# Optimization experiments

Measured on AMD Instinct MI355X. Metric: run time of the kernel, lower is better.

The kernel has to match this reference:

```python
import jax, jax.numpy as jnp
import numpy as np

B, S, OBS, H, A, L = 512, 512, 64, 128, 9, 2
LN_EPS = 1e-5


def setup_inputs() -> dict:
    key = jax.random.key(0)
    ks = jax.random.split(key, 32)
    sc = 0.05
    inp = {
        'obs': jax.random.normal(ks[0], (B, S, OBS), jnp.float32),
        'masks': (jax.random.uniform(ks[1], (B, S)) > 0.01).astype(jnp.float32),
        'noise': jax.random.normal(ks[2], (B, S, A), jnp.float32),
        # encoder: Linear(OBS,H) -> LayerNorm(H) -> ReLU -> Linear(H,H) -> ReLU
        'enc_w1': jax.random.normal(ks[3], (H, OBS)) * sc,
        'enc_b1': jnp.zeros((H,)),
        'ln_g': jnp.ones((H,)),
        'ln_b': jnp.zeros((H,)),
        'enc_w2': jax.random.normal(ks[4], (H, H)) * sc,
        'enc_b2': jnp.zeros((H,)),
        # 2-layer LSTM, torch gate order [i, f, g, o]
        'wih0': jax.random.normal(ks[5], (4 * H, H)) * sc,
        'whh0': jax.random.normal(ks[6], (4 * H, H)) * sc,
        'bih0': jnp.zeros((4 * H,)),
        'bhh0': jnp.zeros((4 * H,)),
        'wih1': jax.random.normal(ks[7], (4 * H, H)) * sc,
        'whh1': jax.random.normal(ks[8], (4 * H, H)) * sc,
        'bih1': jnp.zeros((4 * H,)),
        'bhh1': jnp.zeros((4 * H,)),
        # actor mean head: Linear(H,H//2) -> ReLU -> Linear(H//2,A) -> Tanh
        'am_w1': jax.random.normal(ks[9], (H // 2, H)) * sc,
        'am_b1': jnp.zeros((H // 2,)),
        'am_w2': jax.random.normal(ks[10], (A, H // 2)) * sc,
        'am_b2': jnp.zeros((A,)),
        'log_std': jnp.full((A,), -1.0, jnp.float32),
        # critic head: Linear(H,H//2) -> ReLU -> Linear(H//2,1)
        'cr_w1': jax.random.normal(ks[11], (H // 2, H)) * sc,
        'cr_b1': jnp.zeros((H // 2,)),
        'cr_w2': jax.random.normal(ks[12], (1, H // 2)) * sc,
        'cr_b2': jnp.zeros((1,)),
    }
    return inp


def _encoder(x, w1, b1, g, b, w2, b2):
    y = x @ w1.T + b1
    mu = y.mean(-1, keepdims=True)
    var = y.var(-1, keepdims=True)
    y = (y - mu) * jax.lax.rsqrt(var + LN_EPS) * g + b
    y = jax.nn.relu(y)
    return jax.nn.relu(y @ w2.T + b2)


def _masked_lstm(enc, masks, wih, whh, bih, bhh):
    # enc: (B,S,H), masks: (B,S). Carry h,c: (L,B,H). Reset h,c by mask, then step.
    h0 = jnp.zeros((L, enc.shape[0], H), enc.dtype)
    c0 = jnp.zeros_like(h0)

    def step(carry, xs):
        h, c = carry
        x_t, m_t = xs  # (B,H), (B,1)
        h = h * m_t
        c = c * m_t
        hs, cs = [], []
        inp = x_t
        for l in range(L):
            gates = inp @ wih[l].T + bih[l] + h[l] @ whh[l].T + bhh[l]
            i, f, g, o = jnp.split(gates, 4, axis=-1)
            c_l = jax.nn.sigmoid(f) * c[l] + jax.nn.sigmoid(i) * jnp.tanh(g)
            h_l = jax.nn.sigmoid(o) * jnp.tanh(c_l)
            hs.append(h_l)
            cs.append(c_l)
            inp = h_l
        return (jnp.stack(hs), jnp.stack(cs)), inp

    xs = (enc.transpose(1, 0, 2), masks.T[:, :, None])  # time-major
    (h, c), outs = jax.lax.scan(step, (h0, c0), xs)
    return outs.transpose(1, 0, 2), h, c  # (B,S,H)


def reference(obs, masks, noise, enc_w1, enc_b1, ln_g, ln_b, enc_w2, enc_b2,
              wih0, whh0, bih0, bhh0, wih1, whh1, bih1, bhh1,
              am_w1, am_b1, am_w2, am_b2, log_std, cr_w1, cr_b1, cr_w2, cr_b2):
    enc = _encoder(obs, enc_w1, enc_b1, ln_g, ln_b, enc_w2, enc_b2)
    lstm_out, h, c = _masked_lstm(enc, masks, (wih0, wih1), (whh0, whh1),
                                  (bih0, bih1), (bhh0, bhh1))
    mean = jnp.tanh(jax.nn.relu(lstm_out @ am_w1.T + am_b1) @ am_w2.T + am_b2)
    ls = jnp.clip(log_std, -4.0, 0.0)
    std = jnp.exp(ls)
    action = jax.lax.stop_gradient(mean + std * noise)  # dist.sample()
    z = (action - mean) / std
    log_prob = (-0.5 * z * z - ls - 0.5 * jnp.log(2.0 * jnp.pi)).sum(-1)
    value = (jax.nn.relu(lstm_out @ cr_w1.T + cr_b1) @ cr_w2.T + cr_b2)[..., 0]
    return action, log_prob, value, h, c
```

## Files before the change

kernel.cpp:

```cpp
#include <hip/hip_runtime.h>
#include <hip/hip_bf16.h>
#include <math.h>


#define DEV __device__ __forceinline__

typedef __attribute__((ext_vector_type(4))) float f4;
typedef __attribute__((ext_vector_type(8))) short s16x8;

static constexpr int Bsz = 512, Ssz = 512, OBSD = 64, HD = 128, AD = 9;
static constexpr int TOK = Bsz * Ssz;

static constexpr size_t LP_OFF  = (size_t)TOK * AD;
static constexpr size_t VAL_OFF = LP_OFF + TOK;
static constexpr size_t H_OFF   = VAL_OFF + TOK;
static constexpr size_t C_OFF   = H_OFF + 2 * Bsz * HD;

static constexpr size_t WS_SEQ   = 0;
static constexpr size_t WS_WIH1B = (size_t)TOK * HD * 2;
static constexpr size_t WS_AMW1B = WS_WIH1B + 512 * 128 * 2;
static constexpr size_t WS_AMW2P = WS_AMW1B + 64 * 128 * 2;
static constexpr size_t WS_CRW1B = WS_AMW2P + 16 * 64 * 2;
static constexpr size_t WS_CRW2P = WS_CRW1B + 64 * 128 * 2;

DEV unsigned short f2bf(float f) {
  union { float f; unsigned u; } v; v.f = f;
  unsigned r = v.u + 0x7fffu + ((v.u >> 16) & 1u);
  return (unsigned short)(r >> 16);
}
DEV s16x8 cvt8(f4 a, f4 b) {
  s16x8 r;
  r[0]=(short)f2bf(a[0]); r[1]=(short)f2bf(a[1]); r[2]=(short)f2bf(a[2]); r[3]=(short)f2bf(a[3]);
  r[4]=(short)f2bf(b[0]); r[5]=(short)f2bf(b[1]); r[6]=(short)f2bf(b[2]); r[7]=(short)f2bf(b[3]);
  return r;
}
DEV f4 splat4(float v) { f4 r = {v, v, v, v}; return r; }
DEV f4 mfma16(s16x8 a, s16x8 b, f4 c) {
  return __builtin_amdgcn_mfma_f32_16x16x32_bf16(a, b, c, 0, 0, 0);
}
DEV float fexp2(float x) { return __builtin_amdgcn_exp2f(x); }
DEV float frcp(float x)  { return __builtin_amdgcn_rcpf(x); }
DEV float sigm(float x)   { return frcp(1.f + fexp2(-1.4426950408889634f * x)); }
DEV float tanh_f(float x) { return 2.f * frcp(1.f + fexp2(-2.8853900817779268f * x)) - 1.f; }

__global__ void k_prep(const float* __restrict__ wih1, const float* __restrict__ amw1,
                       const float* __restrict__ amw2, const float* __restrict__ crw1,
                       const float* __restrict__ crw2,
                       unsigned short* __restrict__ wih1b, unsigned short* __restrict__ amw1b,
                       unsigned short* __restrict__ amw2p, unsigned short* __restrict__ crw1b,
                       unsigned short* __restrict__ crw2p)
{
  int i = blockIdx.x * 256 + threadIdx.x;
  if (i < 65536) wih1b[i] = f2bf(wih1[i]);
  if (i < 8192) { amw1b[i] = f2bf(amw1[i]); crw1b[i] = f2bf(crw1[i]); }
  if (i < 1024) {
    int n = i >> 6, k = i & 63;
    amw2p[i] = (n < 9) ? f2bf(amw2[n * 64 + k]) : (unsigned short)0;
    crw2p[i] = (n == 0) ? f2bf(crw2[k]) : (unsigned short)0;
  }
}

__global__ __launch_bounds__(256) void k_encoder(
    const float* __restrict__ obs,
    const float* __restrict__ w1, const float* __restrict__ b1,
    const float* __restrict__ lng, const float* __restrict__ lnb,
    const float* __restrict__ w2, const float* __restrict__ b2,
    unsigned short* __restrict__ enc)
{
  __shared__ unsigned short sy[4][2048];
  const int tid = threadIdx.x, lane = tid & 63, wv = tid >> 6;
  const int cl = lane & 15, grp = lane >> 4;
  const size_t tok0 = ((size_t)blockIdx.x * 4 + wv) * 16;

  s16x8 aob[2];
  {
    const float* p = obs + (tok0 + cl) * 64 + grp * 8;
    aob[0] = cvt8(*(const f4*)p, *(const f4*)(p + 4));
    aob[1] = cvt8(*(const f4*)(p + 32), *(const f4*)(p + 36));
  }

  f4 acc[8];
#pragma unroll
  for (int n = 0; n < 8; ++n) acc[n] = splat4(0.f);
#pragma unroll
  for (int kk = 0; kk < 2; ++kk)
#pragma unroll
    for (int n = 0; n < 8; ++n) {
      const float* p = w1 + (size_t)(n * 16 + cl) * 64 + kk * 32 + grp * 8;
      acc[n] = mfma16(aob[kk], cvt8(*(const f4*)p, *(const f4*)(p + 4)), acc[n]);
    }

  float y[8][4], s[4] = {0,0,0,0}, q[4] = {0,0,0,0};
#pragma unroll
  for (int n = 0; n < 8; ++n) {
    float bb = b1[n * 16 + cl];
#pragma unroll
    for (int i = 0; i < 4; ++i) { float v = acc[n][i] + bb; y[n][i] = v; s[i] += v; q[i] += v * v; }
  }
#pragma unroll
  for (int i = 0; i < 4; ++i)
    for (int m = 1; m < 16; m <<= 1) { s[i] += __shfl_xor(s[i], m); q[i] += __shfl_xor(q[i], m); }
  float mean[4], rstd[4];
#pragma unroll
  for (int i = 0; i < 4; ++i) {
    mean[i] = s[i] * (1.f / 128.f);
    float var = q[i] * (1.f / 128.f) - mean[i] * mean[i];
    rstd[i] = rsqrtf(var + 1e-5f);
  }
  unsigned short* my = sy[wv];
#pragma unroll
  for (int n = 0; n < 8; ++n) {
    float gg = lng[n * 16 + cl], bb = lnb[n * 16 + cl];
#pragma unroll
    for (int i = 0; i < 4; ++i) {
      float v = (y[n][i] - mean[i]) * rstd[i] * gg + bb;
      v = v > 0.f ? v : 0.f;
      int row = grp * 4 + i;
      *(unsigned short*)((char*)my + row * 256 + (((n * 16 + cl) * 2) ^ ((row & 7) << 4))) = f2bf(v);
    }
  }
  __syncthreads();

  f4 acc2[8];
#pragma unroll
  for (int n = 0; n < 8; ++n) acc2[n] = splat4(0.f);
#pragma unroll
  for (int kk = 0; kk < 4; ++kk) {
    s16x8 a2 = *(const s16x8*)((char*)my + cl * 256 + ((kk * 64 + grp * 16) ^ ((cl & 7) << 4)));
#pragma unroll
    for (int n = 0; n < 8; ++n) {
      const float* p = w2 + (size_t)(n * 16 + cl) * 128 + kk * 32 + grp * 8;
      acc2[n] = mfma16(a2, cvt8(*(const f4*)p, *(const f4*)(p + 4)), acc2[n]);
    }
  }
#pragma unroll
  for (int n = 0; n < 8; ++n) {
    float bb = b2[n * 16 + cl];
#pragma unroll
    for (int i = 0; i < 4; ++i) {
      float v = acc2[n][i] + bb; v = v > 0.f ? v : 0.f;
      enc[(tok0 + grp * 4 + i) * 128 + n * 16 + cl] = f2bf(v);
    }
  }
}

__global__ __launch_bounds__(512, 2) void k_lstm(
    const unsigned short* enc_in,
    unsigned short* lstm_out,
    const float* __restrict__ masks,
    const float* __restrict__ wih0f, const float* __restrict__ whh0f,
    const float* __restrict__ bih0, const float* __restrict__ bhh0,
    const unsigned short* __restrict__ wih1b, const float* __restrict__ whh1f,
    const float* __restrict__ bih1, const float* __restrict__ bhh1,
    float* __restrict__ out_h, float* __restrict__ out_c)
{
  extern __shared__ char sm[];
  char* s_h0 = sm + 131072;
  char* s_h1 = sm + 135168;
  unsigned short* s_mk = (unsigned short*)(sm + 139264);

  const int tid = threadIdx.x, lane = tid & 63, wv = tid >> 6;
  const int cl = lane & 15, grp = lane >> 4;
  const int b0 = blockIdx.x * 16, u0 = wv * 16;
  const s16x8 z8 = {0,0,0,0,0,0,0,0};

  for (int idx = tid; idx < 8192; idx += 512) {
    int row = idx >> 4, c8 = idx & 15;
    const float* p = wih0f + (size_t)row * 128 + c8 * 8;
    s16x8 v = cvt8(*(const f4*)p, *(const f4*)(p + 4));
    *(s16x8*)(sm + row * 256 + ((c8 * 16) ^ ((row & 7) << 4))) = v;
  }
  for (int idx = tid; idx < 2048; idx += 512) { ((unsigned short*)s_h0)[idx] = 0; ((unsigned short*)s_h1)[idx] = 0; }
  for (int idx = tid; idx < 8192; idx += 512) {
    int t = idx >> 4, r = idx & 15;
    s_mk[idx] = (masks[(size_t)(b0 + r) * 512 + t] != 0.f) ? 1u : 0u;
  }

  s16x8 Bh0[4][4], Bh1[4][4];
#pragma unroll
  for (int g = 0; g < 4; ++g)
#pragma unroll
    for (int kk = 0; kk < 4; ++kk) {
      const float* p0 = whh0f + (size_t)(g * 128 + u0 + cl) * 128 + kk * 32 + grp * 8;
      Bh0[g][kk] = cvt8(*(const f4*)p0, *(const f4*)(p0 + 4));
      const float* p1 = whh1f + (size_t)(g * 128 + u0 + cl) * 128 + kk * 32 + grp * 8;
      Bh1[g][kk] = cvt8(*(const f4*)p1, *(const f4*)(p1 + 4));
    }
  float bias0[4], bias1[4];
#pragma unroll
  for (int g = 0; g < 4; ++g) {
    bias0[g] = bih0[g * 128 + u0 + cl] + bhh0[g * 128 + u0 + cl];
    bias1[g] = bih1[g * 128 + u0 + cl] + bhh1[g * 128 + u0 + cl];
  }
  float c0[4] = {0,0,0,0}, c1[4] = {0,0,0,0};
  float h0r[4] = {0,0,0,0}, h1r[4] = {0,0,0,0};

  const int swz = (cl & 7) << 4;
  int hoff[4];
#pragma unroll
  for (int kk = 0; kk < 4; ++kk) hoff[kk] = cl * 256 + ((kk * 64 + grp * 16) ^ swz);
  const char* w0l = sm + (u0 + cl) * 256;
  const unsigned short* encl = enc_in + (size_t)(b0 + cl) * 65536 + grp * 8;
  const unsigned short* w1l = wih1b + (size_t)(u0 + cl) * 128 + grp * 8;

  __syncthreads();

  for (int t = 0; t < 512; ++t) {
    const int mA = s_mk[t * 16 + cl];
    float mc[4];
#pragma unroll
    for (int i = 0; i < 4; ++i) mc[i] = s_mk[t * 16 + grp * 4 + i] ? 1.f : 0.f;

    f4 acc[4];
#pragma unroll
    for (int g = 0; g < 4; ++g) acc[g] = splat4(bias0[g]);
#pragma unroll
    for (int kk = 0; kk < 4; ++kk) {
      s16x8 ax = *(const s16x8*)(encl + (size_t)t * 128 + kk * 32);
      s16x8 ah = *(const s16x8*)(s_h0 + hoff[kk]);
      if (!mA) ah = z8;
#pragma unroll
      for (int g = 0; g < 4; ++g) {
        s16x8 bw = *(const s16x8*)(w0l + g * 32768 + ((kk * 64 + grp * 16) ^ swz));
        acc[g] = mfma16(ax, bw, acc[g]);
        acc[g] = mfma16(ah, Bh0[g][kk], acc[g]);
      }
    }
#pragma unroll
    for (int i = 0; i < 4; ++i) {
      float ig = sigm(acc[0][i]), fg = sigm(acc[1][i]);
      float gg = tanh_f(acc[2][i]), og = sigm(acc[3][i]);
      float c = fg * (c0[i] * mc[i]) + ig * gg;
      c0[i] = c; h0r[i] = og * tanh_f(c);
    }
    __syncthreads();
#pragma unroll
    for (int i = 0; i < 4; ++i) {
      int row = grp * 4 + i;
      *(unsigned short*)(s_h0 + row * 256 + (((u0 + cl) * 2) ^ ((row & 7) << 4))) = f2bf(h0r[i]);
    }
    __syncthreads();

#pragma unroll
    for (int g = 0; g < 4; ++g) acc[g] = splat4(bias1[g]);
    s16x8 ax1[4], ah1[4];
#pragma unroll
    for (int kk = 0; kk < 4; ++kk) {
      ax1[kk] = *(const s16x8*)(s_h0 + hoff[kk]);
      ah1[kk] = *(const s16x8*)(s_h1 + hoff[kk]);
      if (!mA) ah1[kk] = z8;
    }
#pragma unroll
    for (int g = 0; g < 4; ++g) {
#pragma unroll
      for (int kk = 0; kk < 4; ++kk) {
        s16x8 bx = *(const s16x8*)(w1l + g * 16384 + kk * 32);
        acc[g] = mfma16(ax1[kk], bx, acc[g]);
        acc[g] = mfma16(ah1[kk], Bh1[g][kk], acc[g]);
      }
    }
#pragma unroll
    for (int i = 0; i < 4; ++i) {
      float ig = sigm(acc[0][i]), fg = sigm(acc[1][i]);
      float gg = tanh_f(acc[2][i]), og = sigm(acc[3][i]);
      float c = fg * (c1[i] * mc[i]) + ig * gg;
      c1[i] = c; h1r[i] = og * tanh_f(c);
    }
    __syncthreads();
#pragma unroll
    for (int i = 0; i < 4; ++i) {
      int row = grp * 4 + i;
      unsigned short hb = f2bf(h1r[i]);
      *(unsigned short*)(s_h1 + row * 256 + (((u0 + cl) * 2) ^ ((row & 7) << 4))) = hb;
      lstm_out[(size_t)(b0 + row) * 65536 + (size_t)t * 128 + u0 + cl] = hb;
    }
    __syncthreads();
  }

#pragma unroll
  for (int i = 0; i < 4; ++i) {
    size_t b = (size_t)b0 + grp * 4 + i;
    out_h[b * 128 + u0 + cl]         = h0r[i];
    out_h[65536 + b * 128 + u0 + cl] = h1r[i];
    out_c[b * 128 + u0 + cl]         = c0[i];
    out_c[65536 + b * 128 + u0 + cl] = c1[i];
  }
}

__global__ __launch_bounds__(256) void k_heads(
    const unsigned short* __restrict__ lo,
    const float* __restrict__ noise,
    const unsigned short* __restrict__ amw1b, const float* __restrict__ am_b1,
    const unsigned short* __restrict__ amw2p, const float* __restrict__ am_b2,
    const float* __restrict__ log_std,
    const unsigned short* __restrict__ crw1b, const float* __restrict__ cr_b1,
    const unsigned short* __restrict__ crw2p, const float* __restrict__ cr_b2,
    float* __restrict__ out)
{
  __shared__ unsigned short sha[4][1024];
  __shared__ unsigned short shc[4][1024];
  const int tid = threadIdx.x, lane = tid & 63, wv = tid >> 6;
  const int cl = lane & 15, grp = lane >> 4;
  const size_t tok0 = ((size_t)blockIdx.x * 4 + wv) * 16;

  s16x8 a[4];
  {
    const unsigned short* p = lo + (tok0 + cl) * 128 + grp * 8;
#pragma unroll
    for (int kk = 0; kk < 4; ++kk) a[kk] = *(const s16x8*)(p + kk * 32);
  }

  f4 acc[4], accc[4];
#pragma unroll
  for (int n = 0; n < 4; ++n) { acc[n] = splat4(0.f); accc[n] = splat4(0.f); }
#pragma unroll
  for (int kk = 0; kk < 4; ++kk)
#pragma unroll
    for (int n = 0; n < 4; ++n) {
      acc[n]  = mfma16(a[kk], *(const s16x8*)(amw1b + (size_t)(n * 16 + cl) * 128 + kk * 32 + grp * 8), acc[n]);
      accc[n] = mfma16(a[kk], *(const s16x8*)(crw1b + (size_t)(n * 16 + cl) * 128 + kk * 32 + grp * 8), accc[n]);
    }
#pragma unroll
  for (int n = 0; n < 4; ++n) {
    float ba = am_b1[n * 16 + cl], bc = cr_b1[n * 16 + cl];
#pragma unroll
    for (int i = 0; i < 4; ++i) {
      int row = grp * 4 + i;
      int off = row * 128 + (((n * 16 + cl) * 2) ^ ((row & 7) << 4));
      float va = acc[n][i] + ba;  va = va > 0.f ? va : 0.f;
      float vc = accc[n][i] + bc; vc = vc > 0.f ? vc : 0.f;
      *(unsigned short*)((char*)sha[wv] + off) = f2bf(va);
      *(unsigned short*)((char*)shc[wv] + off) = f2bf(vc);
    }
  }
  __syncthreads();

  f4 am = splat4(0.f), vv = splat4(0.f);
#pragma unroll
  for (int kk = 0; kk < 2; ++kk) {
    int off = cl * 128 + ((kk * 64 + grp * 16) ^ ((cl & 7) << 4));
    s16x8 a2 = *(const s16x8*)((char*)sha[wv] + off);
    s16x8 c2 = *(const s16x8*)((char*)shc[wv] + off);
    am = mfma16(a2, *(const s16x8*)(amw2p + (size_t)cl * 64 + kk * 32 + grp * 8), am);
    vv = mfma16(c2, *(const s16x8*)(crw2p + (size_t)cl * 64 + kk * 32 + grp * 8), vv);
  }

  float ls = 0.f, stdv = 0.f, b2a = 0.f;
  if (cl < 9) {
    float l = log_std[cl];
    ls = fminf(fmaxf(l, -4.f), 0.f);
    stdv = fexp2(ls * 1.4426950408889634f);
    b2a = am_b2[cl];
  }
  float crb2 = cr_b2[0];
#pragma unroll
  for (int i = 0; i < 4; ++i) {
    size_t tok = tok0 + grp * 4 + i;
    float lp = 0.f;
    if (cl < 9) {
      float meanv = tanh_f(am[i] + b2a);
      float nz = noise[tok * 9 + cl];
      float act = meanv + stdv * nz;
      float z = (act - meanv) / stdv;
      lp = -0.5f * z * z - ls - 0.91893853320467274f;
      out[tok * 9 + cl] = act;
    }
#pragma unroll
    for (int m = 1; m < 16; m <<= 1) lp += __shfl_xor(lp, m);
    if (cl == 0) {
      out[LP_OFF + tok]  = lp;
      out[VAL_OFF + tok] = vv[i] + crb2;
    }
  }
}

extern "C" void kernel_launch(void* const* d_in, const int* in_sizes, int n_in,
                              void* d_out, int out_size, void* d_ws, size_t ws_size,
                              hipStream_t stream)
{
  const float* obs     = (const float*)d_in[0];
  const float* masks   = (const float*)d_in[1];
  const float* noise   = (const float*)d_in[2];
  const float* enc_w1  = (const float*)d_in[3];
  const float* enc_b1  = (const float*)d_in[4];
  const float* ln_g    = (const float*)d_in[5];
  const float* ln_b    = (const float*)d_in[6];
  const float* enc_w2  = (const float*)d_in[7];
  const float* enc_b2  = (const float*)d_in[8];
  const float* wih0    = (const float*)d_in[9];
  const float* whh0    = (const float*)d_in[10];
  const float* bih0    = (const float*)d_in[11];
  const float* bhh0    = (const float*)d_in[12];
  const float* wih1    = (const float*)d_in[13];
  const float* whh1    = (const float*)d_in[14];
  const float* bih1    = (const float*)d_in[15];
  const float* bhh1    = (const float*)d_in[16];
  const float* am_w1   = (const float*)d_in[17];
  const float* am_b1   = (const float*)d_in[18];
  const float* am_w2   = (const float*)d_in[19];
  const float* am_b2   = (const float*)d_in[20];
  const float* log_std = (const float*)d_in[21];
  const float* cr_w1   = (const float*)d_in[22];
  const float* cr_b1   = (const float*)d_in[23];
  const float* cr_w2   = (const float*)d_in[24];
  const float* cr_b2   = (const float*)d_in[25];

  char* ws = (char*)d_ws;
  unsigned short* seq   = (unsigned short*)(ws + WS_SEQ);
  unsigned short* wih1b = (unsigned short*)(ws + WS_WIH1B);
  unsigned short* amw1b = (unsigned short*)(ws + WS_AMW1B);
  unsigned short* amw2p = (unsigned short*)(ws + WS_AMW2P);
  unsigned short* crw1b = (unsigned short*)(ws + WS_CRW1B);
  unsigned short* crw2p = (unsigned short*)(ws + WS_CRW2P);
  float* out            = (float*)d_out;

  hipFuncSetAttribute((const void*)k_lstm, hipFuncAttributeMaxDynamicSharedMemorySize, 155648);

  k_prep<<<256, 256, 0, stream>>>(wih1, am_w1, am_w2, cr_w1, cr_w2,
                                  wih1b, amw1b, amw2p, crw1b, crw2p);
  k_encoder<<<4096, 256, 0, stream>>>(obs, enc_w1, enc_b1, ln_g, ln_b, enc_w2, enc_b2, seq);
  k_lstm<<<32, 512, 155648, stream>>>(seq, seq, masks, wih0, whh0, bih0, bhh0,
                                      wih1b, whh1, bih1, bhh1, out + H_OFF, out + C_OFF);
  k_heads<<<4096, 256, 0, stream>>>(seq, noise, amw1b, am_b1, amw2p, am_b2, log_std,
                                    crw1b, cr_b1, crw2p, cr_b2, out);
}
```

Measured before the change: 3.101 ms.

## Double-buffer LSTM hidden state to halve barriers and prefetch encoder input

The LSTM kernel now keeps h0 and h1 in ping-pong shared-memory buffers indexed by timestep parity, which removes two of the four block barriers per step. The next step's encoder input is prefetched into registers one step ahead, and layer-1 input weights are loaded before the layer-0 gate math so their latency is hidden. The masks are packed into a per-timestep bitmask. lstm_out is now written one step late from the previous h1 buffer using coalesced 8-byte stores. In exchange the kernel uses more registers and a slightly different shared-memory layout, and it relies on the ping-pong order being correct for the recurrence.

```diff
diff --git a/kernel.cpp b/kernel.cpp
--- a/kernel.cpp
+++ b/kernel.cpp
@@ -22,6 +22,11 @@
 static constexpr size_t WS_AMW2P = WS_AMW1B + 64 * 128 * 2;
 static constexpr size_t WS_CRW1B = WS_AMW2P + 16 * 64 * 2;
 static constexpr size_t WS_CRW2P = WS_CRW1B + 64 * 128 * 2;
+
+static constexpr int L_H0  = 131072;
+static constexpr int L_H1  = 139264;
+static constexpr int L_MKB = 147456;
+static constexpr int L_TOT = 149504;
 
 DEV unsigned short f2bf(float f) {
   union { float f; unsigned u; } v; v.f = f;
@@ -155,9 +160,7 @@
     float* __restrict__ out_h, float* __restrict__ out_c)
 {
   extern __shared__ char sm[];
-  char* s_h0 = sm + 131072;
-  char* s_h1 = sm + 135168;
-  unsigned short* s_mk = (unsigned short*)(sm + 139264);
+  unsigned int* s_mkb = (unsigned int*)(sm + L_MKB);
 
   const int tid = threadIdx.x, lane = tid & 63, wv = tid >> 6;
   const int cl = lane & 15, grp = lane >> 4;
@@ -170,10 +173,15 @@
     s16x8 v = cvt8(*(const f4*)p, *(const f4*)(p + 4));
     *(s16x8*)(sm + row * 256 + ((c8 * 16) ^ ((row & 7) << 4))) = v;
   }
-  for (int idx = tid; idx < 2048; idx += 512) { ((unsigned short*)s_h0)[idx] = 0; ((unsigned short*)s_h1)[idx] = 0; }
-  for (int idx = tid; idx < 8192; idx += 512) {
-    int t = idx >> 4, r = idx & 15;
-    s_mk[idx] = (masks[(size_t)(b0 + r) * 512 + t] != 0.f) ? 1u : 0u;
+  for (int idx = tid; idx < 4096; idx += 512)
+    ((unsigned int*)(sm + L_H0))[idx] = 0;
+  {
+    int t = tid;
+    unsigned int m = 0;
+#pragma unroll
+    for (int r = 0; r < 16; ++r)
+      m |= (masks[(size_t)(b0 + r) * 512 + t] != 0.f ? 1u : 0u) << r;
+    s_mkb[t] = m;
   }
 
   s16x8 Bh0[4][4], Bh1[4][4];
@@ -203,29 +211,66 @@
   const unsigned short* encl = enc_in + (size_t)(b0 + cl) * 65536 + grp * 8;
   const unsigned short* w1l = wih1b + (size_t)(u0 + cl) * 128 + grp * 8;
 
+  const int srow = tid >> 5, sj = tid & 31;
+  const int sdso = srow * 256 + ((sj * 8) ^ ((srow & 7) << 4));
+  unsigned short* souts = lstm_out + (size_t)(b0 + srow) * 65536 + sj * 4;
+
   __syncthreads();
 
+  s16x8 axc[4];
+#pragma unroll
+  for (int kk = 0; kk < 4; ++kk) axc[kk] = *(const s16x8*)(encl + kk * 32);
+
   for (int t = 0; t < 512; ++t) {
-    const int mA = s_mk[t * 16 + cl];
+    const int par = t & 1;
+    char* h0p = sm + L_H0 + (par ^ 1) * 4096;
+    char* h0c = sm + L_H0 + par * 4096;
+    char* h1p = sm + L_H1 + (par ^ 1) * 4096;
+    char* h1c = sm + L_H1 + par * 4096;
+
+    if (t > 0) {
+      unsigned long long v = *(const unsigned long long*)(h1p + sdso);
+      *(unsigned long long*)(souts + (size_t)(t - 1) * 128) = v;
+    }
+
+    s16x8 axn[4];
+    {
+      const unsigned short* pe = encl + (size_t)(t + (t < 511 ? 1 : 0)) * 128;
+#pragma unroll
+      for (int kk = 0; kk < 4; ++kk) axn[kk] = *(const s16x8*)(pe + kk * 32);
+    }
+
+    const unsigned int mk = s_mkb[t];
+    const int mA = (mk >> cl) & 1;
     float mc[4];
 #pragma unroll
-    for (int i = 0; i < 4; ++i) mc[i] = s_mk[t * 16 + grp * 4 + i] ? 1.f : 0.f;
+    for (int i = 0; i < 4; ++i) mc[i] = (mk >> (grp * 4 + i)) & 1 ? 1.f : 0.f;
 
     f4 acc[4];
 #pragma unroll
     for (int g = 0; g < 4; ++g) acc[g] = splat4(bias0[g]);
+    s16x8 ah[4];
 #pragma unroll
     for (int kk = 0; kk < 4; ++kk) {
-      s16x8 ax = *(const s16x8*)(encl + (size_t)t * 128 + kk * 32);
-      s16x8 ah = *(const s16x8*)(s_h0 + hoff[kk]);
-      if (!mA) ah = z8;
+      ah[kk] = *(const s16x8*)(h0p + hoff[kk]);
+      if (!mA) ah[kk] = z8;
+    }
+#pragma unroll
+    for (int kk = 0; kk < 4; ++kk)
 #pragma unroll
       for (int g = 0; g < 4; ++g) {
         s16x8 bw = *(const s16x8*)(w0l + g * 32768 + ((kk * 64 + grp * 16) ^ swz));
-        acc[g] = mfma16(ax, bw, acc[g]);
-        acc[g] = mfma16(ah, Bh0[g][kk], acc[g]);
+        acc[g] = mfma16(axc[kk], bw, acc[g]);
+        acc[g] = mfma16(ah[kk], Bh0[g][kk], acc[g]);
       }
-    }
+
+    s16x8 bx1[4][4];
+#pragma unroll
+    for (int g = 0; g < 4; ++g)
+#pragma unroll
+      for (int kk = 0; kk < 4; ++kk)
+        bx1[g][kk] = *(const s16x8*)(w1l + g * 16384 + kk * 32);
+
 #pragma unroll
     for (int i = 0; i < 4; ++i) {
       float ig = sigm(acc[0][i]), fg = sigm(acc[1][i]);
@@ -233,11 +278,10 @@
       float c = fg * (c0[i] * mc[i]) + ig * gg;
       c0[i] = c; h0r[i] = og * tanh_f(c);
     }
-    __syncthreads();
 #pragma unroll
     for (int i = 0; i < 4; ++i) {
       int row = grp * 4 + i;
-      *(unsigned short*)(s_h0 + row * 256 + (((u0 + cl) * 2) ^ ((row & 7) << 4))) = f2bf(h0r[i]);
+      *(unsigned short*)(h0c + row * 256 + (((u0 + cl) * 2) ^ ((row & 7) << 4))) = f2bf(h0r[i]);
     }
     __syncthreads();
 
@@ -246,19 +290,17 @@
     s16x8 ax1[4], ah1[4];
 #pragma unroll
     for (int kk = 0; kk < 4; ++kk) {
-      ax1[kk] = *(const s16x8*)(s_h0 + hoff[kk]);
-      ah1[kk] = *(const s16x8*)(s_h1 + hoff[kk]);
+      ax1[kk] = *(const s16x8*)(h0c + hoff[kk]);
+      ah1[kk] = *(const s16x8*)(h1p + hoff[kk]);
       if (!mA) ah1[kk] = z8;
     }
 #pragma unroll
-    for (int g = 0; g < 4; ++g) {
+    for (int g = 0; g < 4; ++g)
 #pragma unroll
       for (int kk = 0; kk < 4; ++kk) {
-        s16x8 bx = *(const s16x8*)(w1l + g * 16384 + kk * 32);
-        acc[g] = mfma16(ax1[kk], bx, acc[g]);
+        acc[g] = mfma16(ax1[kk], bx1[g][kk], acc[g]);
         acc[g] = mfma16(ah1[kk], Bh1[g][kk], acc[g]);
       }
-    }
 #pragma unroll
     for (int i = 0; i < 4; ++i) {
       float ig = sigm(acc[0][i]), fg = sigm(acc[1][i]);
@@ -266,15 +308,19 @@
       float c = fg * (c1[i] * mc[i]) + ig * gg;
       c1[i] = c; h1r[i] = og * tanh_f(c);
     }
+#pragma unroll
+    for (int i = 0; i < 4; ++i) {
+      int row = grp * 4 + i;
+      *(unsigned short*)(h1c + row * 256 + (((u0 + cl) * 2) ^ ((row & 7) << 4))) = f2bf(h1r[i]);
+    }
+#pragma unroll
+    for (int kk = 0; kk < 4; ++kk) axc[kk] = axn[kk];
     __syncthreads();
-#pragma unroll
-    for (int i = 0; i < 4; ++i) {
-      int row = grp * 4 + i;
-      unsigned short hb = f2bf(h1r[i]);
-      *(unsigned short*)(s_h1 + row * 256 + (((u0 + cl) * 2) ^ ((row & 7) << 4))) = hb;
-      lstm_out[(size_t)(b0 + row) * 65536 + (size_t)t * 128 + u0 + cl] = hb;
-    }
-    __syncthreads();
+  }
+
+  {
+    unsigned long long v = *(const unsigned long long*)(sm + L_H1 + 4096 + sdso);
+    *(unsigned long long*)(souts + (size_t)511 * 128) = v;
   }
 
 #pragma unroll
@@ -414,13 +460,13 @@
   unsigned short* crw2p = (unsigned short*)(ws + WS_CRW2P);
   float* out            = (float*)d_out;
 
-  hipFuncSetAttribute((const void*)k_lstm, hipFuncAttributeMaxDynamicSharedMemorySize, 155648);
+  hipFuncSetAttribute((const void*)k_lstm, hipFuncAttributeMaxDynamicSharedMemorySize, L_TOT);
 
   k_prep<<<256, 256, 0, stream>>>(wih1, am_w1, am_w2, cr_w1, cr_w2,
                                   wih1b, amw1b, amw2p, crw1b, crw2p);
   k_encoder<<<4096, 256, 0, stream>>>(obs, enc_w1, enc_b1, ln_g, ln_b, enc_w2, enc_b2, seq);
-  k_lstm<<<32, 512, 155648, stream>>>(seq, seq, masks, wih0, whh0, bih0, bhh0,
-                                      wih1b, whh1, bih1, bhh1, out + H_OFF, out + C_OFF);
+  k_lstm<<<32, 512, L_TOT, stream>>>(seq, seq, masks, wih0, whh0, bih0, bhh0,
+                                     wih1b, whh1, bih1, bhh1, out + H_OFF, out + C_OFF);
   k_heads<<<4096, 256, 0, stream>>>(seq, noise, amw1b, am_b1, amw2p, am_b2, log_std,
                                     crw1b, cr_b1, crw2p, cr_b2, out);
 }
```

Result: faster. 2.659 ms (-14.3%).
